# Kernel optimization log

Measured on AMD Instinct MI355X. Metric: run time of the kernel, lower is better.

The kernel has to match this reference:

```python
import jax, jax.numpy as jnp
import numpy as np

B, S, D = 4, 1024, 1024
H, DK, DV = 16, 64, 64
EPS = 1e-5

def setup_inputs() -> dict:
    key = jax.random.key(0)
    ks = jax.random.split(key, 13)
    sc = lambda n: 1.0 / np.sqrt(n)
    return {
        "Q": jax.random.normal(ks[0], (B, S, D), jnp.float32),
        "K": jax.random.normal(ks[1], (B, S, D), jnp.float32),
        "V": jax.random.normal(ks[2], (B, S, D), jnp.float32),
        "Wq": jax.random.normal(ks[3], (D, H * DK), jnp.float32) * sc(D),
        "bq": jax.random.normal(ks[4], (H * DK,), jnp.float32) * 0.01,
        "Wk": jax.random.normal(ks[5], (D, H * DK), jnp.float32) * sc(D),
        "bk": jax.random.normal(ks[6], (H * DK,), jnp.float32) * 0.01,
        "Wv": jax.random.normal(ks[7], (D, H * DV), jnp.float32) * sc(D),
        "bv": jax.random.normal(ks[8], (H * DV,), jnp.float32) * 0.01,
        "Wo": jax.random.normal(ks[9], (H * DV, D), jnp.float32) * sc(H * DV),
        "bo": jax.random.normal(ks[10], (D,), jnp.float32) * 0.01,
        "pos_k": jax.random.normal(ks[11], (H * S, DK), jnp.float32) * 0.02,
        "pos_v": jax.random.normal(ks[12], (H * S, DV), jnp.float32) * 0.02,
        "gamma": jnp.ones((D,), jnp.float32),
        "beta": jnp.zeros((D,), jnp.float32),
    }

def reference(Q, K, V, Wq, bq, Wk, bk, Wv, bv, Wo, bo, pos_k, pos_v, gamma, beta):
    b = Q.shape[0]
    # projections + head split: [b, h, s, dk/dv]
    q = (Q @ Wq + bq).reshape(b, S, H, DK).transpose(0, 2, 1, 3)
    k = (K @ Wk + bk).reshape(b, S, H, DK).transpose(0, 2, 1, 3)
    v = (V @ Wv + bv).reshape(b, S, H, DV).transpose(0, 2, 1, 3)
    # pos_ids = arange(H*S).view(1, H, S) -> embedding lookup is just a reshape
    K_pos = pos_k.reshape(1, H, S, DK)
    V_pos = pos_v.reshape(1, H, S, DV)
    scores = jnp.einsum("bhqd,bhkd->bhqk", q, k + K_pos) / np.sqrt(DK).astype(np.float32)
    attn = jax.nn.softmax(scores, axis=-1)
    context = jnp.einsum("bhqk,bhkd->bhqd", attn, v + V_pos)
    context = context.transpose(0, 2, 1, 3).reshape(b, S, H * DV)
    out = context @ Wo + bo + Q  # residual
    mu = jnp.mean(out, axis=-1, keepdims=True)
    var = jnp.var(out, axis=-1, keepdims=True)
    out = (out - mu) * jax.lax.rsqrt(var + EPS) * gamma + beta
    return (out, attn)
```

## Files before the change

kernel.cpp:

```cpp
#include <hip/hip_runtime.h>
#include <cstdint>
#include <cstddef>


typedef __attribute__((ext_vector_type(8))) short short8;
typedef __attribute__((ext_vector_type(4))) short short4v;
typedef __attribute__((ext_vector_type(4))) float f32x4;

typedef __attribute__((address_space(1))) void gl_void;
typedef __attribute__((address_space(3))) void lds_void;

#define MFMA16(a, b, c) __builtin_amdgcn_mfma_f32_16x16x32_bf16(a, b, c, 0, 0, 0)

__device__ __forceinline__ unsigned short f2bf(float f) {
  union { float f; unsigned u; } v; v.f = f;
  unsigned r = v.u + 0x7FFFu + ((v.u >> 16) & 1u);
  return (unsigned short)(r >> 16);
}
__device__ __forceinline__ float bf2f(unsigned short h) {
  union { unsigned u; float f; } v; v.u = ((unsigned)h) << 16;
  return v.f;
}

__global__ __launch_bounds__(256) void transpose_w(
    const float* __restrict__ wq, const float* __restrict__ wk,
    const float* __restrict__ wv, const float* __restrict__ wo,
    unsigned short* __restrict__ wt) {
  __shared__ unsigned short tile[64][68];
  const int z = blockIdx.z;
  const float* W = (z == 0) ? wq : (z == 1) ? wk : (z == 2) ? wv : wo;
  unsigned short* out = wt + (size_t)z * 1048576;
  const int n0 = blockIdx.x * 64, k0 = blockIdx.y * 64;
  const int tr = threadIdx.x >> 4;
  const int tc = (threadIdx.x & 15) * 4;
#pragma unroll
  for (int i = 0; i < 4; ++i) {
    int k = tr + i * 16;
    float4 x = *reinterpret_cast<const float4*>(W + (size_t)(k0 + k) * 1024 + n0 + tc);
    tile[k][tc + 0] = f2bf(x.x); tile[k][tc + 1] = f2bf(x.y);
    tile[k][tc + 2] = f2bf(x.z); tile[k][tc + 3] = f2bf(x.w);
  }
  __syncthreads();
#pragma unroll
  for (int i = 0; i < 4; ++i) {
    int n = tr + i * 16;
    short4v o;
    o[0] = (short)tile[tc + 0][n]; o[1] = (short)tile[tc + 1][n];
    o[2] = (short)tile[tc + 2][n]; o[3] = (short)tile[tc + 3][n];
    *reinterpret_cast<short4v*>(out + (size_t)(n0 + n) * 1024 + k0 + tc) = o;
  }
}

__global__ __launch_bounds__(256) void gemm_qkv(
    const float* __restrict__ Qf, const float* __restrict__ Kf,
    const float* __restrict__ Vf, const unsigned short* __restrict__ wt,
    const float* __restrict__ bq, const float* __restrict__ bk,
    const float* __restrict__ bv, const float* __restrict__ pos_k,
    const float* __restrict__ pos_v, unsigned short* __restrict__ qb,
    unsigned short* __restrict__ kbuf, unsigned short* __restrict__ vT) {
  __shared__ unsigned short lds[16384];
  const int z = blockIdx.z;
  const float* A = (z == 0) ? Qf : (z == 1) ? Kf : Vf;
  const unsigned short* Bt = wt + (size_t)z * 1048576;
  const float* bias = (z == 0) ? bq : (z == 1) ? bk : bv;

  const int tid = threadIdx.x;
  const int lane = tid & 63;
  const int w = tid >> 6;
  const int g = lane >> 4;
  const int lr = lane & 15;
  const int wg = blockIdx.y * 8 + blockIdx.x;
  const int lg = (wg & 7) * 32 + (wg >> 3);
  const int m0 = (lg >> 3) << 7;
  const int n0 = (lg & 7) << 7;
  const int wm = w >> 1, wn = w & 1;

  const int ra0 = tid >> 2, ca = tid & 3;
  const int ra1 = ra0 + 64;
  const int wA0 = ra0 * 64 + ((ca ^ ((ra0 >> 1) & 3)) << 4);
  const int wA1 = ra1 * 64 + ((ca ^ ((ra1 >> 1) & 3)) << 4);
  const float* a0p = A + (size_t)(m0 + ra0) * 1024 + ca * 8;
  const float* a1p = A + (size_t)(m0 + ra1) * 1024 + ca * 8;

  const int c0 = (w << 6) + lane;
  const int r0 = c0 >> 2;
  const int sl0 = (c0 & 3) ^ ((r0 >> 1) & 3);
  const int c1 = c0 + 256;
  const int r1 = c1 >> 2;
  const int sl1 = (c1 & 3) ^ ((r1 >> 1) & 3);
  const size_t gb0 = ((size_t)(n0 + r0) << 10) + (sl0 << 3);
  const size_t gb1 = ((size_t)(n0 + r1) << 10) + (sl1 << 3);
  char* ldsc = (char*)lds;

  int offA[4], offB[4];
#pragma unroll
  for (int i = 0; i < 4; ++i) {
    int rt = (wm << 6) + (i << 4) + lr;
    offA[i] = rt * 64 + ((g ^ ((rt >> 1) & 3)) << 4);
    int nt = (wn << 6) + (i << 4) + lr;
    offB[i] = nt * 64 + ((g ^ ((nt >> 1) & 3)) << 4);
  }

  f32x4 acc[4][4] = {};

  {
    const float4 fa = *reinterpret_cast<const float4*>(a0p);
    const float4 fb = *reinterpret_cast<const float4*>(a0p + 4);
    const float4 fc = *reinterpret_cast<const float4*>(a1p);
    const float4 fd = *reinterpret_cast<const float4*>(a1p + 4);
    short8 pa, pb;
    pa[0] = (short)f2bf(fa.x); pa[1] = (short)f2bf(fa.y);
    pa[2] = (short)f2bf(fa.z); pa[3] = (short)f2bf(fa.w);
    pa[4] = (short)f2bf(fb.x); pa[5] = (short)f2bf(fb.y);
    pa[6] = (short)f2bf(fb.z); pa[7] = (short)f2bf(fb.w);
    pb[0] = (short)f2bf(fc.x); pb[1] = (short)f2bf(fc.y);
    pb[2] = (short)f2bf(fc.z); pb[3] = (short)f2bf(fc.w);
    pb[4] = (short)f2bf(fd.x); pb[5] = (short)f2bf(fd.y);
    pb[6] = (short)f2bf(fd.z); pb[7] = (short)f2bf(fd.w);
    *reinterpret_cast<short8*>(ldsc + wA0) = pa;
    *reinterpret_cast<short8*>(ldsc + wA1) = pb;
    __builtin_amdgcn_global_load_lds((gl_void*)(Bt + gb0),
                                     (lds_void*)(ldsc + 16384 + (w << 10)), 16, 0, 0);
    __builtin_amdgcn_global_load_lds((gl_void*)(Bt + gb1),
                                     (lds_void*)(ldsc + 16384 + 4096 + (w << 10)), 16, 0, 0);
    __syncthreads();
  }

  for (int kt = 0; kt < 32; ++kt) {
    const int cur = (kt & 1) << 13;
    const int nxt = ((kt + 1) & 1) << 13;
    float4 fa, fb, fc, fd;
    if (kt < 31) {
      const int kb32 = (kt + 1) << 5;
      __builtin_amdgcn_global_load_lds((gl_void*)(Bt + gb0 + kb32),
                                       (lds_void*)(ldsc + 16384 + nxt + (w << 10)), 16, 0, 0);
      __builtin_amdgcn_global_load_lds((gl_void*)(Bt + gb1 + kb32),
                                       (lds_void*)(ldsc + 16384 + nxt + 4096 + (w << 10)), 16, 0, 0);
      fa = *reinterpret_cast<const float4*>(a0p + kb32);
      fb = *reinterpret_cast<const float4*>(a0p + kb32 + 4);
      fc = *reinterpret_cast<const float4*>(a1p + kb32);
      fd = *reinterpret_cast<const float4*>(a1p + kb32 + 4);
    }
    short8 am[4], bn[4];
#pragma unroll
    for (int i = 0; i < 4; ++i) {
      am[i] = *reinterpret_cast<const short8*>(ldsc + cur + offA[i]);
      bn[i] = *reinterpret_cast<const short8*>(ldsc + 16384 + cur + offB[i]);
    }
#pragma unroll
    for (int i = 0; i < 4; ++i)
#pragma unroll
      for (int j = 0; j < 4; ++j)
        acc[i][j] = MFMA16(am[i], bn[j], acc[i][j]);
    if (kt < 31) {
      short8 pa, pb;
      pa[0] = (short)f2bf(fa.x); pa[1] = (short)f2bf(fa.y);
      pa[2] = (short)f2bf(fa.z); pa[3] = (short)f2bf(fa.w);
      pa[4] = (short)f2bf(fb.x); pa[5] = (short)f2bf(fb.y);
      pa[6] = (short)f2bf(fb.z); pa[7] = (short)f2bf(fb.w);
      pb[0] = (short)f2bf(fc.x); pb[1] = (short)f2bf(fc.y);
      pb[2] = (short)f2bf(fc.z); pb[3] = (short)f2bf(fc.w);
      pb[4] = (short)f2bf(fd.x); pb[5] = (short)f2bf(fd.y);
      pb[6] = (short)f2bf(fd.z); pb[7] = (short)f2bf(fd.w);
      *reinterpret_cast<short8*>(ldsc + nxt + wA0) = pa;
      *reinterpret_cast<short8*>(ldsc + nxt + wA1) = pb;
    }
    __syncthreads();
  }

#pragma unroll
  for (int i = 0; i < 4; ++i) {
#pragma unroll
    for (int j = 0; j < 4; ++j) {
      const int n = n0 + (wn << 6) + (j << 4) + lr;
      const int hh = n >> 6, dk = n & 63;
      const float bs = bias[n];
      const int mb = m0 + (wm << 6) + (i << 4) + (g << 2);
      const int b = mb >> 10, s0 = mb & 1023;
      if (z == 2) {
        short4v o;
#pragma unroll
        for (int r = 0; r < 4; ++r) {
          const float val = acc[i][j][r] + bs +
                            pos_v[((((size_t)hh << 10) + s0 + r) << 6) + dk];
          o[r] = (short)f2bf(val);
        }
        *reinterpret_cast<short4v*>(
            vT + ((size_t)((b * 16 + hh) * 64 + dk) << 10) + s0) = o;
      } else {
#pragma unroll
        for (int r = 0; r < 4; ++r) {
          float val = acc[i][j][r];
          if (z == 0) {
            val = (val + bs) * 0.125f;
          } else {
            val = val + bs + pos_k[((((size_t)hh << 10) + s0 + r) << 6) + dk];
          }
          unsigned short* dst = (z == 0) ? qb : kbuf;
          dst[((((size_t)(b * 16 + hh) << 10) + s0 + r) << 6) + dk] = f2bf(val);
        }
      }
    }
  }
}

__global__ __launch_bounds__(256) void rowsum_kernel(
    const unsigned short* __restrict__ qb,
    const unsigned short* __restrict__ kb,
    float* __restrict__ l_out) {
  __shared__ char smem[16384];
  const int tid = threadIdx.x;
  const int lane = tid & 63;
  const int w = tid >> 6;
  const int g = lane >> 4;
  const int lr = lane & 15;
  const int wg = ((blockIdx.x & 7) << 7) + (blockIdx.x >> 3);
  const int bh = wg >> 4, qt = wg & 15;
  const int qrow0 = (qt << 6) + (w << 4);
  const size_t headoff = (size_t)bh << 16;

  const size_t qoff = headoff + (size_t)(qrow0 + lr) * 64 + (g << 3);
  const short8 a0 = *reinterpret_cast<const short8*>(qb + qoff);
  const short8 a1 = *reinterpret_cast<const short8*>(qb + qoff + 32);

  const int key0 = tid >> 3, sl0 = (tid & 7) ^ (key0 & 7);
  const int key1 = 32 + (tid >> 3), sl1 = (tid & 7) ^ (key1 & 7);
  const unsigned short* src0 = kb + headoff + (size_t)key0 * 64 + (sl0 << 3);
  const unsigned short* src1 = kb + headoff + (size_t)key1 * 64 + (sl1 << 3);

  __builtin_amdgcn_global_load_lds((gl_void*)src0,
                                   (lds_void*)(smem + (w << 10)), 16, 0, 0);
  __builtin_amdgcn_global_load_lds((gl_void*)src1,
                                   (lds_void*)(smem + 4096 + (w << 10)), 16, 0, 0);
  __syncthreads();

  float l[4] = {0.f, 0.f, 0.f, 0.f};
  for (int ct = 0; ct < 16; ++ct) {
    const int cur = (ct & 1) << 13;
    if (ct < 15) {
      const int nxt = ((ct + 1) & 1) << 13;
      const int koff = (ct + 1) << 12;
      __builtin_amdgcn_global_load_lds((gl_void*)(src0 + koff),
                                       (lds_void*)(smem + nxt + (w << 10)), 16, 0, 0);
      __builtin_amdgcn_global_load_lds((gl_void*)(src1 + koff),
                                       (lds_void*)(smem + nxt + 4096 + (w << 10)), 16, 0, 0);
    }
    const char* kl = smem + cur;
#pragma unroll
    for (int kf = 0; kf < 4; ++kf) {
      const int kr = (kf << 4) + lr;
      const char* row = kl + (kr << 7);
      const short8 b0 = *reinterpret_cast<const short8*>(row + ((g ^ (kr & 7)) << 4));
      const short8 b1 = *reinterpret_cast<const short8*>(row + (((4 + g) ^ (kr & 7)) << 4));
      f32x4 acc = {0.f, 0.f, 0.f, 0.f};
      acc = MFMA16(a0, b0, acc);
      acc = MFMA16(a1, b1, acc);
#pragma unroll
      for (int r = 0; r < 4; ++r) l[r] += __expf(acc[r]);
    }
    __syncthreads();
  }
#pragma unroll
  for (int r = 0; r < 4; ++r) {
    l[r] += __shfl_xor(l[r], 1);
    l[r] += __shfl_xor(l[r], 2);
    l[r] += __shfl_xor(l[r], 4);
    l[r] += __shfl_xor(l[r], 8);
  }
  if (lr == 0) {
#pragma unroll
    for (int r = 0; r < 4; ++r)
      l_out[((size_t)bh << 10) + qrow0 + (g << 2) + r] = l[r];
  }
}

__global__ __launch_bounds__(256) void attn_pv_kernel(
    const unsigned short* __restrict__ qb,
    const unsigned short* __restrict__ kb,
    const unsigned short* __restrict__ vT,
    const float* __restrict__ l_in,
    unsigned short* __restrict__ ctxb,
    float* __restrict__ attn_out) {
  __shared__ char smem[40960];
  const int tid = threadIdx.x;
  const int lane = tid & 63;
  const int w = tid >> 6;
  const int g = lane >> 4;
  const int lr = lane & 15;
  const int wg = ((blockIdx.x & 7) << 7) + (blockIdx.x >> 3);
  const int bh = wg >> 4, qt = wg & 15;
  const int b = bh >> 4, h = bh & 15;
  const int qrow0 = (qt << 6) + (w << 4);
  const size_t headoff = (size_t)bh << 16;

  const size_t qoff = headoff + (size_t)(qrow0 + lr) * 64 + (g << 3);
  const short8 a0 = *reinterpret_cast<const short8*>(qb + qoff);
  const short8 a1 = *reinterpret_cast<const short8*>(qb + qoff + 32);

  float inv[4];
#pragma unroll
  for (int r = 0; r < 4; ++r)
    inv[r] = 1.0f / l_in[((size_t)bh << 10) + qrow0 + (g << 2) + r];

  const int key0 = tid >> 3, sl0 = (tid & 7) ^ (key0 & 7);
  const int key1 = 32 + (tid >> 3), sl1 = (tid & 7) ^ (key1 & 7);
  const unsigned short* ks0 = kb + headoff + (size_t)key0 * 64 + (sl0 << 3);
  const unsigned short* ks1 = kb + headoff + (size_t)key1 * 64 + (sl1 << 3);
  const unsigned short* vs0 = vT + headoff + ((size_t)key0 << 10) + (sl0 << 3);
  const unsigned short* vs1 = vT + headoff + ((size_t)key1 << 10) + (sl1 << 3);

  char* ew = smem + 32768 + (w << 11);
  float* ab = attn_out + ((size_t)bh << 20);
  f32x4 ctx[4] = {};

  __builtin_amdgcn_global_load_lds((gl_void*)ks0,
                                   (lds_void*)(smem + (w << 10)), 16, 0, 0);
  __builtin_amdgcn_global_load_lds((gl_void*)ks1,
                                   (lds_void*)(smem + 4096 + (w << 10)), 16, 0, 0);
  __builtin_amdgcn_global_load_lds((gl_void*)vs0,
                                   (lds_void*)(smem + 16384 + (w << 10)), 16, 0, 0);
  __builtin_amdgcn_global_load_lds((gl_void*)vs1,
                                   (lds_void*)(smem + 16384 + 4096 + (w << 10)), 16, 0, 0);
  __syncthreads();

  for (int ct = 0; ct < 16; ++ct) {
    const int cur = (ct & 1) << 13;
    const int kc0 = ct << 6;
    if (ct < 15) {
      const int nxt = ((ct + 1) & 1) << 13;
      const int kn = (ct + 1) << 6;
      __builtin_amdgcn_global_load_lds((gl_void*)(ks0 + ((size_t)kn << 6)),
                                       (lds_void*)(smem + nxt + (w << 10)), 16, 0, 0);
      __builtin_amdgcn_global_load_lds((gl_void*)(ks1 + ((size_t)kn << 6)),
                                       (lds_void*)(smem + nxt + 4096 + (w << 10)), 16, 0, 0);
      __builtin_amdgcn_global_load_lds((gl_void*)(vs0 + kn),
                                       (lds_void*)(smem + 16384 + nxt + (w << 10)), 16, 0, 0);
      __builtin_amdgcn_global_load_lds((gl_void*)(vs1 + kn),
                                       (lds_void*)(smem + 16384 + nxt + 4096 + (w << 10)), 16, 0, 0);
    }
    const char* kl = smem + cur;
    const char* vl = smem + 16384 + cur;

#pragma unroll
    for (int kf = 0; kf < 4; ++kf) {
      const int kr = (kf << 4) + lr;
      const char* row = kl + (kr << 7);
      const short8 b0 = *reinterpret_cast<const short8*>(row + ((g ^ (kr & 7)) << 4));
      const short8 b1 = *reinterpret_cast<const short8*>(row + (((4 + g) ^ (kr & 7)) << 4));
      f32x4 acc = {0.f, 0.f, 0.f, 0.f};
      acc = MFMA16(a0, b0, acc);
      acc = MFMA16(a1, b1, acc);
#pragma unroll
      for (int r = 0; r < 4; ++r) {
        const float p = __expf(acc[r]) * inv[r];
        const int prow = (g << 2) + r;
        const int kc = (kf << 4) + lr;
        *(unsigned short*)(ew + (prow << 7) + ((((kc >> 3) ^ (prow & 7))) << 4) +
                           ((kc & 7) << 1)) = f2bf(p);
      }
    }

#pragma unroll
    for (int p2 = 0; p2 < 2; ++p2) {
      const int row = lane >> 2;
      const int s = (lane & 3) + (p2 << 2);
      const short8 pv = *reinterpret_cast<const short8*>(
          ew + (row << 7) + ((s ^ (row & 7)) << 4));
      float* dst = ab + ((size_t)(qrow0 + row) << 10) + kc0 + (s << 3);
      float4 o0, o1;
      o0.x = bf2f((unsigned short)pv[0]); o0.y = bf2f((unsigned short)pv[1]);
      o0.z = bf2f((unsigned short)pv[2]); o0.w = bf2f((unsigned short)pv[3]);
      o1.x = bf2f((unsigned short)pv[4]); o1.y = bf2f((unsigned short)pv[5]);
      o1.z = bf2f((unsigned short)pv[6]); o1.w = bf2f((unsigned short)pv[7]);
      *reinterpret_cast<float4*>(dst) = o0;
      *reinterpret_cast<float4*>(dst + 4) = o1;
    }

    const short8 pa0 = *reinterpret_cast<const short8*>(
        ew + (lr << 7) + ((g ^ (lr & 7)) << 4));
    const short8 pa1 = *reinterpret_cast<const short8*>(
        ew + (lr << 7) + (((4 + g) ^ (lr & 7)) << 4));
#pragma unroll
    for (int dt = 0; dt < 4; ++dt) {
      const int dv = (dt << 4) + lr;
      const char* vrow = vl + (dv << 7);
      const short8 v0 = *reinterpret_cast<const short8*>(vrow + ((g ^ (dv & 7)) << 4));
      const short8 v1 = *reinterpret_cast<const short8*>(vrow + (((4 + g) ^ (dv & 7)) << 4));
      ctx[dt] = MFMA16(pa0, v0, ctx[dt]);
      ctx[dt] = MFMA16(pa1, v1, ctx[dt]);
    }
    __syncthreads();
  }

#pragma unroll
  for (int dt = 0; dt < 4; ++dt) {
#pragma unroll
    for (int r = 0; r < 4; ++r) {
      const int srow = qrow0 + (g << 2) + r;
      const int n = (h << 6) + (dt << 4) + lr;
      ctxb[((((size_t)(b << 10)) + srow) << 10) + n] = f2bf(ctx[dt][r]);
    }
  }
}

__global__ __launch_bounds__(256) void gemm_out(
    const unsigned short* __restrict__ A, const unsigned short* __restrict__ Bt,
    const float* __restrict__ bias, const float* __restrict__ resid,
    float* __restrict__ outf) {
  __shared__ unsigned short lds[16384];
  const int tid = threadIdx.x;
  const int lane = tid & 63;
  const int w = tid >> 6;
  const int g = lane >> 4;
  const int lr = lane & 15;
  const int wg = blockIdx.y * 8 + blockIdx.x;
  const int lg = (wg & 7) * 32 + (wg >> 3);
  const int m0 = (lg >> 3) << 7;
  const int n0 = (lg & 7) << 7;
  const int wm = w >> 1, wn = w & 1;

  const int c0 = (w << 6) + lane;
  const int r0 = c0 >> 2;
  const int sl0 = (c0 & 3) ^ ((r0 >> 1) & 3);
  const int c1 = c0 + 256;
  const int r1 = c1 >> 2;
  const int sl1 = (c1 & 3) ^ ((r1 >> 1) & 3);

  const size_t ga0 = ((size_t)(m0 + r0) << 10) + (sl0 << 3);
  const size_t ga1 = ((size_t)(m0 + r1) << 10) + (sl1 << 3);
  const size_t gb0 = ((size_t)(n0 + r0) << 10) + (sl0 << 3);
  const size_t gb1 = ((size_t)(n0 + r1) << 10) + (sl1 << 3);

  char* ldsc = (char*)lds;

  int offA[4], offB[4];
#pragma unroll
  for (int i = 0; i < 4; ++i) {
    int rt = (wm << 6) + (i << 4) + lr;
    offA[i] = rt * 64 + ((g ^ ((rt >> 1) & 3)) << 4);
    int nt = (wn << 6) + (i << 4) + lr;
    offB[i] = nt * 64 + ((g ^ ((nt >> 1) & 3)) << 4);
  }

  __builtin_amdgcn_global_load_lds((gl_void*)(A + ga0),
                                   (lds_void*)(ldsc + (w << 10)), 16, 0, 0);
  __builtin_amdgcn_global_load_lds((gl_void*)(A + ga1),
                                   (lds_void*)(ldsc + 4096 + (w << 10)), 16, 0, 0);
  __builtin_amdgcn_global_load_lds((gl_void*)(Bt + gb0),
                                   (lds_void*)(ldsc + 16384 + (w << 10)), 16, 0, 0);
  __builtin_amdgcn_global_load_lds((gl_void*)(Bt + gb1),
                                   (lds_void*)(ldsc + 16384 + 4096 + (w << 10)), 16, 0, 0);
  __syncthreads();

  f32x4 acc[4][4] = {};
  for (int kt = 0; kt < 32; ++kt) {
    const int cur = (kt & 1) << 13;
    if (kt < 31) {
      const int nxt = ((kt + 1) & 1) << 13;
      const int kb32 = (kt + 1) << 5;
      __builtin_amdgcn_global_load_lds((gl_void*)(A + ga0 + kb32),
                                       (lds_void*)(ldsc + nxt + (w << 10)), 16, 0, 0);
      __builtin_amdgcn_global_load_lds((gl_void*)(A + ga1 + kb32),
                                       (lds_void*)(ldsc + nxt + 4096 + (w << 10)), 16, 0, 0);
      __builtin_amdgcn_global_load_lds((gl_void*)(Bt + gb0 + kb32),
                                       (lds_void*)(ldsc + 16384 + nxt + (w << 10)), 16, 0, 0);
      __builtin_amdgcn_global_load_lds((gl_void*)(Bt + gb1 + kb32),
                                       (lds_void*)(ldsc + 16384 + nxt + 4096 + (w << 10)), 16, 0, 0);
    }
    short8 am[4], bn[4];
#pragma unroll
    for (int i = 0; i < 4; ++i) {
      am[i] = *reinterpret_cast<const short8*>(ldsc + cur + offA[i]);
      bn[i] = *reinterpret_cast<const short8*>(ldsc + 16384 + cur + offB[i]);
    }
#pragma unroll
    for (int i = 0; i < 4; ++i)
#pragma unroll
      for (int j = 0; j < 4; ++j)
        acc[i][j] = MFMA16(am[i], bn[j], acc[i][j]);
    __syncthreads();
  }

#pragma unroll
  for (int i = 0; i < 4; ++i) {
#pragma unroll
    for (int j = 0; j < 4; ++j) {
      const int n = n0 + (wn << 6) + (j << 4) + lr;
      const float bs = bias[n];
#pragma unroll
      for (int r = 0; r < 4; ++r) {
        const int m = m0 + (wm << 6) + (i << 4) + (g << 2) + r;
        outf[((size_t)m << 10) + n] =
            acc[i][j][r] + bs + resid[((size_t)m << 10) + n];
      }
    }
  }
}

__global__ __launch_bounds__(256) void layernorm_kernel(
    const float* __restrict__ x, const float* __restrict__ gamma,
    const float* __restrict__ beta, float* __restrict__ out) {
  __shared__ float red[8];
  const int row = blockIdx.x, t = threadIdx.x;
  const float4 v = *reinterpret_cast<const float4*>(x + ((size_t)row << 10) + t * 4);
  float s1 = v.x + v.y + v.z + v.w;
  float s2 = v.x * v.x + v.y * v.y + v.z * v.z + v.w * v.w;
#pragma unroll
  for (int off = 1; off < 64; off <<= 1) {
    s1 += __shfl_xor(s1, off);
    s2 += __shfl_xor(s2, off);
  }
  const int w = t >> 6;
  if ((t & 63) == 0) { red[w * 2] = s1; red[w * 2 + 1] = s2; }
  __syncthreads();
  s1 = red[0] + red[2] + red[4] + red[6];
  s2 = red[1] + red[3] + red[5] + red[7];
  const float mu = s1 * (1.0f / 1024.0f);
  const float var = s2 * (1.0f / 1024.0f) - mu * mu;
  const float rs = rsqrtf(var + 1e-5f);
  const float4 gm = *reinterpret_cast<const float4*>(gamma + t * 4);
  const float4 bt = *reinterpret_cast<const float4*>(beta + t * 4);
  float4 o;
  o.x = (v.x - mu) * rs * gm.x + bt.x;
  o.y = (v.y - mu) * rs * gm.y + bt.y;
  o.z = (v.z - mu) * rs * gm.z + bt.z;
  o.w = (v.w - mu) * rs * gm.w + bt.w;
  *reinterpret_cast<float4*>(out + ((size_t)row << 10) + t * 4) = o;
}

static constexpr size_t OFF_QB = 0;
static constexpr size_t OFF_KB = 8388608;
static constexpr size_t OFF_VT = 16777216;
static constexpr size_t OFF_WT = 25165824;
static constexpr size_t OFF_CTX = 33554432;
static constexpr size_t OFF_LN = 41943040;
static constexpr size_t OFF_L = 58720256;

extern "C" void kernel_launch(void* const* d_in, const int* in_sizes, int n_in,
                              void* d_out, int out_size, void* d_ws, size_t ws_size,
                              hipStream_t stream) {
  (void)in_sizes; (void)n_in; (void)out_size; (void)ws_size;
  const float* Q = (const float*)d_in[0];
  const float* K = (const float*)d_in[1];
  const float* V = (const float*)d_in[2];
  const float* Wq = (const float*)d_in[3];
  const float* bq = (const float*)d_in[4];
  const float* Wk = (const float*)d_in[5];
  const float* bk = (const float*)d_in[6];
  const float* Wv = (const float*)d_in[7];
  const float* bv = (const float*)d_in[8];
  const float* Wo = (const float*)d_in[9];
  const float* bo = (const float*)d_in[10];
  const float* pos_k = (const float*)d_in[11];
  const float* pos_v = (const float*)d_in[12];
  const float* gamma = (const float*)d_in[13];
  const float* beta = (const float*)d_in[14];

  char* ws = (char*)d_ws;
  unsigned short* qb = (unsigned short*)(ws + OFF_QB);
  unsigned short* kb = (unsigned short*)(ws + OFF_KB);
  unsigned short* vT = (unsigned short*)(ws + OFF_VT);
  unsigned short* wt = (unsigned short*)(ws + OFF_WT);
  unsigned short* ctxb = (unsigned short*)(ws + OFF_CTX);
  float* lnb = (float*)(ws + OFF_LN);
  float* lbuf = (float*)(ws + OFF_L);

  float* outF = (float*)d_out;
  float* attnF = outF + 4194304;

  transpose_w<<<dim3(16, 16, 4), 256, 0, stream>>>(Wq, Wk, Wv, Wo, wt);
  gemm_qkv<<<dim3(8, 32, 3), 256, 0, stream>>>(Q, K, V, wt, bq, bk, bv,
                                               pos_k, pos_v, qb, kb, vT);
  rowsum_kernel<<<dim3(1024), 256, 0, stream>>>(qb, kb, lbuf);
  attn_pv_kernel<<<dim3(1024), 256, 0, stream>>>(qb, kb, vT, lbuf, ctxb, attnF);
  gemm_out<<<dim3(8, 32), 256, 0, stream>>>(ctxb, wt + 3145728, bo, Q, lnb);
  layernorm_kernel<<<4096, 256, 0, stream>>>(lnb, gamma, beta, outF);
}
```

Before: 204.3 us.

## Fuse rowsum into attention kernel, deepen LDS prefetch, use exp2 and nontemporal stores

The separate row-sum kernel is merged into the attention kernel, which now runs two passes over K inside one launch and no longer round-trips the softmax denominators through global memory. The GEMM and attention loops switch from a single __syncthreads to explicit vmcnt waits plus s_barrier, so the next-plus-one tile is prefetched into LDS while the current one is computed. The Q scale folds in log2(e) so exp2f replaces __expf. Attention and LayerNorm outputs now use nontemporal stores to reduce cache pollution. The hand-placed waitcnt values are fragile and must exactly match the number of outstanding loads.

Result: slower. 232.3 us (+13.7%).

```diff
diff --git a/kernel.cpp b/kernel.cpp
--- a/kernel.cpp
+++ b/kernel.cpp
@@ -11,6 +11,10 @@
 typedef __attribute__((address_space(3))) void lds_void;
 
 #define MFMA16(a, b, c) __builtin_amdgcn_mfma_f32_16x16x32_bf16(a, b, c, 0, 0, 0)
+#define GLL(src, dst) __builtin_amdgcn_global_load_lds((gl_void*)(src), (lds_void*)(dst), 16, 0, 0)
+#define SBAR() __builtin_amdgcn_s_barrier()
+#define WAIT_VM(n) do { asm volatile("s_waitcnt vmcnt(" #n ")" ::: "memory"); __builtin_amdgcn_sched_barrier(0); } while (0)
+#define WAIT_VM_LGKM(n) do { asm volatile("s_waitcnt vmcnt(" #n ") lgkmcnt(0)" ::: "memory"); __builtin_amdgcn_sched_barrier(0); } while (0)
 
 __device__ __forceinline__ unsigned short f2bf(float f) {
   union { float f; unsigned u; } v; v.f = f;
@@ -108,6 +112,10 @@
     const float4 fb = *reinterpret_cast<const float4*>(a0p + 4);
     const float4 fc = *reinterpret_cast<const float4*>(a1p);
     const float4 fd = *reinterpret_cast<const float4*>(a1p + 4);
+    GLL(Bt + gb0, ldsc + 16384 + (w << 10));
+    GLL(Bt + gb1, ldsc + 16384 + 4096 + (w << 10));
+    GLL(Bt + gb0 + 32, ldsc + 16384 + 8192 + (w << 10));
+    GLL(Bt + gb1 + 32, ldsc + 16384 + 8192 + 4096 + (w << 10));
     short8 pa, pb;
     pa[0] = (short)f2bf(fa.x); pa[1] = (short)f2bf(fa.y);
     pa[2] = (short)f2bf(fa.z); pa[3] = (short)f2bf(fa.w);
@@ -119,23 +127,16 @@
     pb[6] = (short)f2bf(fd.z); pb[7] = (short)f2bf(fd.w);
     *reinterpret_cast<short8*>(ldsc + wA0) = pa;
     *reinterpret_cast<short8*>(ldsc + wA1) = pb;
-    __builtin_amdgcn_global_load_lds((gl_void*)(Bt + gb0),
-                                     (lds_void*)(ldsc + 16384 + (w << 10)), 16, 0, 0);
-    __builtin_amdgcn_global_load_lds((gl_void*)(Bt + gb1),
-                                     (lds_void*)(ldsc + 16384 + 4096 + (w << 10)), 16, 0, 0);
-    __syncthreads();
   }
 
   for (int kt = 0; kt < 32; ++kt) {
     const int cur = (kt & 1) << 13;
     const int nxt = ((kt + 1) & 1) << 13;
+    if (kt < 31) WAIT_VM_LGKM(2); else WAIT_VM_LGKM(0);
+    SBAR();
     float4 fa, fb, fc, fd;
     if (kt < 31) {
       const int kb32 = (kt + 1) << 5;
-      __builtin_amdgcn_global_load_lds((gl_void*)(Bt + gb0 + kb32),
-                                       (lds_void*)(ldsc + 16384 + nxt + (w << 10)), 16, 0, 0);
-      __builtin_amdgcn_global_load_lds((gl_void*)(Bt + gb1 + kb32),
-                                       (lds_void*)(ldsc + 16384 + nxt + 4096 + (w << 10)), 16, 0, 0);
       fa = *reinterpret_cast<const float4*>(a0p + kb32);
       fb = *reinterpret_cast<const float4*>(a0p + kb32 + 4);
       fc = *reinterpret_cast<const float4*>(a1p + kb32);
@@ -152,6 +153,12 @@
 #pragma unroll
       for (int j = 0; j < 4; ++j)
         acc[i][j] = MFMA16(am[i], bn[j], acc[i][j]);
+    SBAR();
+    if (kt < 30) {
+      const int kb32 = (kt + 2) << 5;
+      GLL(Bt + gb0 + kb32, ldsc + 16384 + cur + (w << 10));
+      GLL(Bt + gb1 + kb32, ldsc + 16384 + cur + 4096 + (w << 10));
+    }
     if (kt < 31) {
       short8 pa, pb;
       pa[0] = (short)f2bf(fa.x); pa[1] = (short)f2bf(fa.y);
@@ -165,7 +172,6 @@
       *reinterpret_cast<short8*>(ldsc + nxt + wA0) = pa;
       *reinterpret_cast<short8*>(ldsc + nxt + wA1) = pb;
     }
-    __syncthreads();
   }
 
 #pragma unroll
@@ -192,7 +198,7 @@
         for (int r = 0; r < 4; ++r) {
           float val = acc[i][j][r];
           if (z == 0) {
-            val = (val + bs) * 0.125f;
+            val = (val + bs) * 0.180336880111f;
           } else {
             val = val + bs + pos_k[((((size_t)hh << 10) + s0 + r) << 6) + dk];
           }
@@ -204,81 +210,10 @@
   }
 }
 
-__global__ __launch_bounds__(256) void rowsum_kernel(
-    const unsigned short* __restrict__ qb,
-    const unsigned short* __restrict__ kb,
-    float* __restrict__ l_out) {
-  __shared__ char smem[16384];
-  const int tid = threadIdx.x;
-  const int lane = tid & 63;
-  const int w = tid >> 6;
-  const int g = lane >> 4;
-  const int lr = lane & 15;
-  const int wg = ((blockIdx.x & 7) << 7) + (blockIdx.x >> 3);
-  const int bh = wg >> 4, qt = wg & 15;
-  const int qrow0 = (qt << 6) + (w << 4);
-  const size_t headoff = (size_t)bh << 16;
-
-  const size_t qoff = headoff + (size_t)(qrow0 + lr) * 64 + (g << 3);
-  const short8 a0 = *reinterpret_cast<const short8*>(qb + qoff);
-  const short8 a1 = *reinterpret_cast<const short8*>(qb + qoff + 32);
-
-  const int key0 = tid >> 3, sl0 = (tid & 7) ^ (key0 & 7);
-  const int key1 = 32 + (tid >> 3), sl1 = (tid & 7) ^ (key1 & 7);
-  const unsigned short* src0 = kb + headoff + (size_t)key0 * 64 + (sl0 << 3);
-  const unsigned short* src1 = kb + headoff + (size_t)key1 * 64 + (sl1 << 3);
-
-  __builtin_amdgcn_global_load_lds((gl_void*)src0,
-                                   (lds_void*)(smem + (w << 10)), 16, 0, 0);
-  __builtin_amdgcn_global_load_lds((gl_void*)src1,
-                                   (lds_void*)(smem + 4096 + (w << 10)), 16, 0, 0);
-  __syncthreads();
-
-  float l[4] = {0.f, 0.f, 0.f, 0.f};
-  for (int ct = 0; ct < 16; ++ct) {
-    const int cur = (ct & 1) << 13;
-    if (ct < 15) {
-      const int nxt = ((ct + 1) & 1) << 13;
-      const int koff = (ct + 1) << 12;
-      __builtin_amdgcn_global_load_lds((gl_void*)(src0 + koff),
-                                       (lds_void*)(smem + nxt + (w << 10)), 16, 0, 0);
-      __builtin_amdgcn_global_load_lds((gl_void*)(src1 + koff),
-                                       (lds_void*)(smem + nxt + 4096 + (w << 10)), 16, 0, 0);
-    }
-    const char* kl = smem + cur;
-#pragma unroll
-    for (int kf = 0; kf < 4; ++kf) {
-      const int kr = (kf << 4) + lr;
-      const char* row = kl + (kr << 7);
-      const short8 b0 = *reinterpret_cast<const short8*>(row + ((g ^ (kr & 7)) << 4));
-      const short8 b1 = *reinterpret_cast<const short8*>(row + (((4 + g) ^ (kr & 7)) << 4));
-      f32x4 acc = {0.f, 0.f, 0.f, 0.f};
-      acc = MFMA16(a0, b0, acc);
-      acc = MFMA16(a1, b1, acc);
-#pragma unroll
-      for (int r = 0; r < 4; ++r) l[r] += __expf(acc[r]);
-    }
-    __syncthreads();
-  }
-#pragma unroll
-  for (int r = 0; r < 4; ++r) {
-    l[r] += __shfl_xor(l[r], 1);
-    l[r] += __shfl_xor(l[r], 2);
-    l[r] += __shfl_xor(l[r], 4);
-    l[r] += __shfl_xor(l[r], 8);
-  }
-  if (lr == 0) {
-#pragma unroll
-    for (int r = 0; r < 4; ++r)
-      l_out[((size_t)bh << 10) + qrow0 + (g << 2) + r] = l[r];
-  }
-}
-
-__global__ __launch_bounds__(256) void attn_pv_kernel(
+__global__ __launch_bounds__(256) void attn_fused(
     const unsigned short* __restrict__ qb,
     const unsigned short* __restrict__ kb,
     const unsigned short* __restrict__ vT,
-    const float* __restrict__ l_in,
     unsigned short* __restrict__ ctxb,
     float* __restrict__ attn_out) {
   __shared__ char smem[40960];
@@ -297,11 +232,6 @@
   const short8 a0 = *reinterpret_cast<const short8*>(qb + qoff);
   const short8 a1 = *reinterpret_cast<const short8*>(qb + qoff + 32);
 
-  float inv[4];
-#pragma unroll
-  for (int r = 0; r < 4; ++r)
-    inv[r] = 1.0f / l_in[((size_t)bh << 10) + qrow0 + (g << 2) + r];
-
   const int key0 = tid >> 3, sl0 = (tid & 7) ^ (key0 & 7);
   const int key1 = 32 + (tid >> 3), sl1 = (tid & 7) ^ (key1 & 7);
   const unsigned short* ks0 = kb + headoff + (size_t)key0 * 64 + (sl0 << 3);
@@ -309,38 +239,16 @@
   const unsigned short* vs0 = vT + headoff + ((size_t)key0 << 10) + (sl0 << 3);
   const unsigned short* vs1 = vT + headoff + ((size_t)key1 << 10) + (sl1 << 3);
 
-  char* ew = smem + 32768 + (w << 11);
-  float* ab = attn_out + ((size_t)bh << 20);
-  f32x4 ctx[4] = {};
-
-  __builtin_amdgcn_global_load_lds((gl_void*)ks0,
-                                   (lds_void*)(smem + (w << 10)), 16, 0, 0);
-  __builtin_amdgcn_global_load_lds((gl_void*)ks1,
-                                   (lds_void*)(smem + 4096 + (w << 10)), 16, 0, 0);
-  __builtin_amdgcn_global_load_lds((gl_void*)vs0,
-                                   (lds_void*)(smem + 16384 + (w << 10)), 16, 0, 0);
-  __builtin_amdgcn_global_load_lds((gl_void*)vs1,
-                                   (lds_void*)(smem + 16384 + 4096 + (w << 10)), 16, 0, 0);
-  __syncthreads();
-
+  GLL(ks0, smem + (w << 10));
+  GLL(ks1, smem + 4096 + (w << 10));
+  GLL(ks0 + 4096, smem + 8192 + (w << 10));
+  GLL(ks1 + 4096, smem + 8192 + 4096 + (w << 10));
+
+  float l[4] = {0.f, 0.f, 0.f, 0.f};
   for (int ct = 0; ct < 16; ++ct) {
-    const int cur = (ct & 1) << 13;
-    const int kc0 = ct << 6;
-    if (ct < 15) {
-      const int nxt = ((ct + 1) & 1) << 13;
-      const int kn = (ct + 1) << 6;
-      __builtin_amdgcn_global_load_lds((gl_void*)(ks0 + ((size_t)kn << 6)),
-                                       (lds_void*)(smem + nxt + (w << 10)), 16, 0, 0);
-      __builtin_amdgcn_global_load_lds((gl_void*)(ks1 + ((size_t)kn << 6)),
-                                       (lds_void*)(smem + nxt + 4096 + (w << 10)), 16, 0, 0);
-      __builtin_amdgcn_global_load_lds((gl_void*)(vs0 + kn),
-                                       (lds_void*)(smem + 16384 + nxt + (w << 10)), 16, 0, 0);
-      __builtin_amdgcn_global_load_lds((gl_void*)(vs1 + kn),
-                                       (lds_void*)(smem + 16384 + nxt + 4096 + (w << 10)), 16, 0, 0);
-    }
-    const char* kl = smem + cur;
-    const char* vl = smem + 16384 + cur;
-
+    if (ct < 15) WAIT_VM(2); else WAIT_VM(0);
+    SBAR();
+    const char* kl = smem + ((ct & 1) << 13);
 #pragma unroll
     for (int kf = 0; kf < 4; ++kf) {
       const int kr = (kf << 4) + lr;
@@ -351,8 +259,62 @@
       acc = MFMA16(a0, b0, acc);
       acc = MFMA16(a1, b1, acc);
 #pragma unroll
+      for (int r = 0; r < 4; ++r) l[r] += exp2f(acc[r]);
+    }
+    SBAR();
+    if (ct + 2 < 16) {
+      const int koff = (ct + 2) << 12;
+      const int bo = (ct & 1) << 13;
+      GLL(ks0 + koff, smem + bo + (w << 10));
+      GLL(ks1 + koff, smem + bo + 4096 + (w << 10));
+    }
+  }
+#pragma unroll
+  for (int r = 0; r < 4; ++r) {
+    l[r] += __shfl_xor(l[r], 1);
+    l[r] += __shfl_xor(l[r], 2);
+    l[r] += __shfl_xor(l[r], 4);
+    l[r] += __shfl_xor(l[r], 8);
+  }
+  float inv[4];
+#pragma unroll
+  for (int r = 0; r < 4; ++r) inv[r] = 1.0f / l[r];
+
+  GLL(ks0, smem + (w << 10));
+  GLL(ks1, smem + 4096 + (w << 10));
+  GLL(vs0, smem + 16384 + (w << 10));
+  GLL(vs1, smem + 16384 + 4096 + (w << 10));
+  GLL(ks0 + 4096, smem + 8192 + (w << 10));
+  GLL(ks1 + 4096, smem + 8192 + 4096 + (w << 10));
+  GLL(vs0 + 64, smem + 16384 + 8192 + (w << 10));
+  GLL(vs1 + 64, smem + 16384 + 8192 + 4096 + (w << 10));
+
+  char* ew = smem + 32768 + (w << 11);
+  float* ab = attn_out + ((size_t)bh << 20);
+  f32x4 ctx[4] = {};
+
+  for (int ct = 0; ct < 16; ++ct) {
+    if (ct == 0) { WAIT_VM(4); }
+    else if (ct == 15) { WAIT_VM(4); }
+    else { WAIT_VM(8); }
+    SBAR();
+    const int cur = (ct & 1) << 13;
+    const int kc0 = ct << 6;
+    const char* kl = smem + cur;
+    const char* vl = smem + 16384 + cur;
+
+#pragma unroll
+    for (int kf = 0; kf < 4; ++kf) {
+      const int kr = (kf << 4) + lr;
+      const char* row = kl + (kr << 7);
+      const short8 b0 = *reinterpret_cast<const short8*>(row + ((g ^ (kr & 7)) << 4));
+      const short8 b1 = *reinterpret_cast<const short8*>(row + (((4 + g) ^ (kr & 7)) << 4));
+      f32x4 acc = {0.f, 0.f, 0.f, 0.f};
+      acc = MFMA16(a0, b0, acc);
+      acc = MFMA16(a1, b1, acc);
+#pragma unroll
       for (int r = 0; r < 4; ++r) {
-        const float p = __expf(acc[r]) * inv[r];
+        const float p = exp2f(acc[r]) * inv[r];
         const int prow = (g << 2) + r;
         const int kc = (kf << 4) + lr;
         *(unsigned short*)(ew + (prow << 7) + ((((kc >> 3) ^ (prow & 7))) << 4) +
@@ -367,13 +329,13 @@
       const short8 pv = *reinterpret_cast<const short8*>(
           ew + (row << 7) + ((s ^ (row & 7)) << 4));
       float* dst = ab + ((size_t)(qrow0 + row) << 10) + kc0 + (s << 3);
-      float4 o0, o1;
-      o0.x = bf2f((unsigned short)pv[0]); o0.y = bf2f((unsigned short)pv[1]);
-      o0.z = bf2f((unsigned short)pv[2]); o0.w = bf2f((unsigned short)pv[3]);
-      o1.x = bf2f((unsigned short)pv[4]); o1.y = bf2f((unsigned short)pv[5]);
-      o1.z = bf2f((unsigned short)pv[6]); o1.w = bf2f((unsigned short)pv[7]);
-      *reinterpret_cast<float4*>(dst) = o0;
-      *reinterpret_cast<float4*>(dst + 4) = o1;
+      f32x4 o0, o1;
+      o0[0] = bf2f((unsigned short)pv[0]); o0[1] = bf2f((unsigned short)pv[1]);
+      o0[2] = bf2f((unsigned short)pv[2]); o0[3] = bf2f((unsigned short)pv[3]);
+      o1[0] = bf2f((unsigned short)pv[4]); o1[1] = bf2f((unsigned short)pv[5]);
+      o1[2] = bf2f((unsigned short)pv[6]); o1[3] = bf2f((unsigned short)pv[7]);
+      __builtin_nontemporal_store(o0, reinterpret_cast<f32x4*>(dst));
+      __builtin_nontemporal_store(o1, reinterpret_cast<f32x4*>(dst + 4));
     }
 
     const short8 pa0 = *reinterpret_cast<const short8*>(
@@ -389,7 +351,15 @@
       ctx[dt] = MFMA16(pa0, v0, ctx[dt]);
       ctx[dt] = MFMA16(pa1, v1, ctx[dt]);
     }
-    __syncthreads();
+    SBAR();
+    if (ct + 2 < 16) {
+      const int kn = (ct + 2) << 6;
+      const int bo = (ct & 1) << 13;
+      GLL(ks0 + ((size_t)kn << 6), smem + bo + (w << 10));
+      GLL(ks1 + ((size_t)kn << 6), smem + bo + 4096 + (w << 10));
+      GLL(vs0 + kn, smem + 16384 + bo + (w << 10));
+      GLL(vs1 + kn, smem + 16384 + bo + 4096 + (w << 10));
+    }
   }
 
 #pragma unroll
@@ -442,31 +412,20 @@
     offB[i] = nt * 64 + ((g ^ ((nt >> 1) & 3)) << 4);
   }
 
-  __builtin_amdgcn_global_load_lds((gl_void*)(A + ga0),
-                                   (lds_void*)(ldsc + (w << 10)), 16, 0, 0);
-  __builtin_amdgcn_global_load_lds((gl_void*)(A + ga1),
-                                   (lds_void*)(ldsc + 4096 + (w << 10)), 16, 0, 0);
-  __builtin_amdgcn_global_load_lds((gl_void*)(Bt + gb0),
-                                   (lds_void*)(ldsc + 16384 + (w << 10)), 16, 0, 0);
-  __builtin_amdgcn_global_load_lds((gl_void*)(Bt + gb1),
-                                   (lds_void*)(ldsc + 16384 + 4096 + (w << 10)), 16, 0, 0);
-  __syncthreads();
+  GLL(A + ga0, ldsc + (w << 10));
+  GLL(A + ga1, ldsc + 4096 + (w << 10));
+  GLL(Bt + gb0, ldsc + 16384 + (w << 10));
+  GLL(Bt + gb1, ldsc + 16384 + 4096 + (w << 10));
+  GLL(A + ga0 + 32, ldsc + 8192 + (w << 10));
+  GLL(A + ga1 + 32, ldsc + 8192 + 4096 + (w << 10));
+  GLL(Bt + gb0 + 32, ldsc + 16384 + 8192 + (w << 10));
+  GLL(Bt + gb1 + 32, ldsc + 16384 + 8192 + 4096 + (w << 10));
 
   f32x4 acc[4][4] = {};
   for (int kt = 0; kt < 32; ++kt) {
+    if (kt < 31) WAIT_VM(4); else WAIT_VM(0);
+    SBAR();
     const int cur = (kt & 1) << 13;
-    if (kt < 31) {
-      const int nxt = ((kt + 1) & 1) << 13;
-      const int kb32 = (kt + 1) << 5;
-      __builtin_amdgcn_global_load_lds((gl_void*)(A + ga0 + kb32),
-                                       (lds_void*)(ldsc + nxt + (w << 10)), 16, 0, 0);
-      __builtin_amdgcn_global_load_lds((gl_void*)(A + ga1 + kb32),
-                                       (lds_void*)(ldsc + nxt + 4096 + (w << 10)), 16, 0, 0);
-      __builtin_amdgcn_global_load_lds((gl_void*)(Bt + gb0 + kb32),
-                                       (lds_void*)(ldsc + 16384 + nxt + (w << 10)), 16, 0, 0);
-      __builtin_amdgcn_global_load_lds((gl_void*)(Bt + gb1 + kb32),
-                                       (lds_void*)(ldsc + 16384 + nxt + 4096 + (w << 10)), 16, 0, 0);
-    }
     short8 am[4], bn[4];
 #pragma unroll
     for (int i = 0; i < 4; ++i) {
@@ -478,7 +437,14 @@
 #pragma unroll
       for (int j = 0; j < 4; ++j)
         acc[i][j] = MFMA16(am[i], bn[j], acc[i][j]);
-    __syncthreads();
+    SBAR();
+    if (kt < 30) {
+      const int kb32 = (kt + 2) << 5;
+      GLL(A + ga0 + kb32, ldsc + cur + (w << 10));
+      GLL(A + ga1 + kb32, ldsc + cur + 4096 + (w << 10));
+      GLL(Bt + gb0 + kb32, ldsc + 16384 + cur + (w << 10));
+      GLL(Bt + gb1 + kb32, ldsc + 16384 + cur + 4096 + (w << 10));
+    }
   }
 
 #pragma unroll
@@ -520,12 +486,12 @@
   const float rs = rsqrtf(var + 1e-5f);
   const float4 gm = *reinterpret_cast<const float4*>(gamma + t * 4);
   const float4 bt = *reinterpret_cast<const float4*>(beta + t * 4);
-  float4 o;
-  o.x = (v.x - mu) * rs * gm.x + bt.x;
-  o.y = (v.y - mu) * rs * gm.y + bt.y;
-  o.z = (v.z - mu) * rs * gm.z + bt.z;
-  o.w = (v.w - mu) * rs * gm.w + bt.w;
-  *reinterpret_cast<float4*>(out + ((size_t)row << 10) + t * 4) = o;
+  f32x4 o;
+  o[0] = (v.x - mu) * rs * gm.x + bt.x;
+  o[1] = (v.y - mu) * rs * gm.y + bt.y;
+  o[2] = (v.z - mu) * rs * gm.z + bt.z;
+  o[3] = (v.w - mu) * rs * gm.w + bt.w;
+  __builtin_nontemporal_store(o, reinterpret_cast<f32x4*>(out + ((size_t)row << 10) + t * 4));
 }
 
 static constexpr size_t OFF_QB = 0;
@@ -534,7 +500,6 @@
 static constexpr size_t OFF_WT = 25165824;
 static constexpr size_t OFF_CTX = 33554432;
 static constexpr size_t OFF_LN = 41943040;
-static constexpr size_t OFF_L = 58720256;
 
 extern "C" void kernel_launch(void* const* d_in, const int* in_sizes, int n_in,
                               void* d_out, int out_size, void* d_ws, size_t ws_size,
@@ -563,7 +528,6 @@
   unsigned short* wt = (unsigned short*)(ws + OFF_WT);
   unsigned short* ctxb = (unsigned short*)(ws + OFF_CTX);
   float* lnb = (float*)(ws + OFF_LN);
-  float* lbuf = (float*)(ws + OFF_L);
 
   float* outF = (float*)d_out;
   float* attnF = outF + 4194304;
@@ -571,8 +535,7 @@
   transpose_w<<<dim3(16, 16, 4), 256, 0, stream>>>(Wq, Wk, Wv, Wo, wt);
   gemm_qkv<<<dim3(8, 32, 3), 256, 0, stream>>>(Q, K, V, wt, bq, bk, bv,
                                                pos_k, pos_v, qb, kb, vT);
-  rowsum_kernel<<<dim3(1024), 256, 0, stream>>>(qb, kb, lbuf);
-  attn_pv_kernel<<<dim3(1024), 256, 0, stream>>>(qb, kb, vT, lbuf, ctxb, attnF);
+  attn_fused<<<dim3(1024), 256, 0, stream>>>(qb, kb, vT, ctxb, attnF);
   gemm_out<<<dim3(8, 32), 256, 0, stream>>>(ctxb, wt + 3145728, bo, Q, lnb);
   layernorm_kernel<<<4096, 256, 0, stream>>>(lnb, gamma, beta, outF);
 }
```
